# Kernel optimization log

Hardware: AMD Instinct MI355X
Metric: run time of the kernel (lower is better)

Reference implementation:

```python
import jax, jax.numpy as jnp
import numpy as np

B = 8192
T = 100       # repeat_vector
I = 30        # input_size
H = 100       # hidden_size


def setup_inputs() -> dict:
    key = jax.random.key(0)
    ks = jax.random.split(key, 7)
    k = 1.0 / np.sqrt(H)  # torch LSTM/Linear init scale
    u = lambda kk, shape: jax.random.uniform(kk, shape, jnp.float32, -k, k)
    return {
        "x": jax.random.normal(ks[0], (B, I), jnp.float32),
        "W_ih": u(ks[1], (4 * H, I)),   # gate order: i, f, g, o
        "W_hh": u(ks[2], (4 * H, H)),
        "b_ih": u(ks[3], (4 * H,)),
        "b_hh": u(ks[4], (4 * H,)),
        "W_d": u(ks[5], (1, H)),
        "b_d": u(ks[6], (1,)),
    }


def _lstm_dense(x, W_ih, W_hh, b_ih, b_hh, W_d, b_d):
    # Input is the same vector at every timestep (repeat), so project once.
    xp = x @ W_ih.T + b_ih + b_hh  # [B, 4H]
    h0 = jnp.zeros((x.shape[0], H), x.dtype)
    c0 = jnp.zeros((x.shape[0], H), x.dtype)

    def step(carry, _):
        h, c = carry
        gates = xp + h @ W_hh.T                      # [B, 4H]
        i, f, g, o = jnp.split(gates, 4, axis=-1)
        i = jax.nn.sigmoid(i)
        f = jax.nn.sigmoid(f)
        g = jnp.tanh(g)
        o = jax.nn.sigmoid(o)
        c = f * c + i * g
        h = o * jnp.tanh(c)
        return (h, c), h

    _, hs = jax.lax.scan(step, (h0, c0), None, length=T)  # [T, B, H]
    hs = jnp.transpose(hs, (1, 0, 2))                     # [B, T, H]
    return hs @ W_d.T + b_d                               # [B, T, 1]


def reference(x, W_ih, W_hh, b_ih, b_hh, W_d, b_d):
    return _lstm_dense(x, W_ih, W_hh, b_ih, b_hh, W_d, b_d)
```

## Files before the change

kernel.cpp:

```cpp
#include <hip/hip_runtime.h>


#define LOG2E 1.44269504088896340736f

typedef _Float16 f16x8 __attribute__((ext_vector_type(8)));
typedef float    f32x4 __attribute__((ext_vector_type(4)));
typedef float    f32x2 __attribute__((ext_vector_type(2)));

__device__ __forceinline__ float rcp_(float x) { return __builtin_amdgcn_rcpf(x); }
__device__ __forceinline__ float exp2_(float x) { return __builtin_amdgcn_exp2f(x); }

#define KS2 168

__global__ __launch_bounds__(448, 4) void lstm_kernel(
    const float* __restrict__ x, const float* __restrict__ Wih,
    const float* __restrict__ Whh, const float* __restrict__ bih,
    const float* __restrict__ bhh, const float* __restrict__ Wd,
    const float* __restrict__ bd, float* __restrict__ out)
{
    __shared__ __align__(16) char smem[128 * KS2 * 2];
    __shared__ __align__(16) _Float16 hlds[2][16 * KS2];

    _Float16* Wstg = (_Float16*)smem;
    float*    outb = (float*)smem;

    const int tid = threadIdx.x;
    const int w   = tid >> 6;
    const int l   = tid & 63;
    const int g   = l >> 4;
    const int c   = l & 15;
    const int b0  = blockIdx.x * 16;
    const int u   = w * 16 + c;
    const bool wpo = (w == 6) && (c == 5);

    for (int i = tid; i < 128 * KS2 / 2; i += 448) ((unsigned*)Wstg)[i] = 0u;
    for (int i = tid; i < 2 * 16 * KS2 / 2; i += 448) ((unsigned*)&hlds[0][0])[i] = 0u;
    __syncthreads();

    for (int idx = tid; idx < 960; idx += 448) {
        int buf = idx / 480, rem = idx - buf * 480;
        int rr = rem / 30, kk = rem - rr * 30;
        hlds[buf][rr * KS2 + 112 + kk] = (_Float16)x[(b0 + rr) * 30 + kk];
    }
    if (tid < 32) hlds[tid >> 4][(tid & 15) * KS2 + 142] = (_Float16)1.0f;

    f16x8 wfrag[4][5];
    for (int s = 0; s < 4; ++s) {
        const float sc = (s == 2) ? (-2.0f * LOG2E) : (-LOG2E);
        for (int idx = tid; idx < 13100; idx += 448) {
            if (idx < 10000) {
                int uu = idx / 100, k = idx - uu * 100;
                Wstg[uu * KS2 + k] = (_Float16)(Whh[(s * 100 + uu) * 100 + k] * sc);
            } else if (idx < 13000) {
                int j = idx - 10000, uu = j / 30, k = j - uu * 30;
                Wstg[uu * KS2 + 112 + k] = (_Float16)(Wih[(s * 100 + uu) * 30 + k] * sc);
            } else {
                int uu = idx - 13000;
                Wstg[uu * KS2 + 142] =
                    (_Float16)((bih[s * 100 + uu] + bhh[s * 100 + uu]) * sc);
            }
        }
        if (s == 0) {
            for (int k = tid; k < 100; k += 448)
                Wstg[101 * KS2 + k] = (_Float16)Wd[k];
            if (tid == 0) Wstg[101 * KS2 + 142] = (_Float16)bd[0];
        }
        __syncthreads();
        #pragma unroll
        for (int ks = 0; ks < 5; ++ks)
            wfrag[s][ks] = *(const f16x8*)&Wstg[u * KS2 + ks * 32 + g * 8];
        __syncthreads();
    }

    f32x2 creg2[2] = {{0.f, 0.f}, {0.f, 0.f}};
    __syncthreads();

    const int afb = c * KS2 + g * 8;

#define STEP(P, TCUR)                                                         \
    {                                                                         \
        const _Float16* hr = &hlds[(P)][0];                                   \
        _Float16*       hw = &hlds[(P) ^ 1][0];                               \
        f32x4 acc[4];                                                         \
        _Pragma("unroll")                                                     \
        for (int s = 0; s < 4; ++s) acc[s] = (f32x4){0.f, 0.f, 0.f, 0.f};     \
        _Pragma("unroll")                                                     \
        for (int ks = 0; ks < 5; ++ks) {                                      \
            f16x8 a = *(const f16x8*)&hr[afb + ks * 32];                      \
            _Pragma("unroll")                                                 \
            for (int s = 0; s < 4; ++s)                                       \
                acc[s] = __builtin_amdgcn_mfma_f32_16x16x32_f16(              \
                        a, wfrag[s][ks], acc[s], 0, 0, 0);                    \
        }                                                                     \
              \
        if ((TCUR) > 0 && wpo) {                                              \
            _Pragma("unroll")                                                 \
            for (int r = 0; r < 4; ++r)                                       \
                outb[(4 * g + r) * 100 + (TCUR) - 1] = acc[0][r];             \
        }                                                                     \
                                   \
        _Pragma("unroll")                                                     \
        for (int q = 0; q < 2; ++q) {                                         \
            f32x2 A2 = {exp2_(acc[0][2 * q]), exp2_(acc[0][2 * q + 1])};      \
            f32x2 F2 = {exp2_(acc[1][2 * q]), exp2_(acc[1][2 * q + 1])};      \
            f32x2 G2 = {exp2_(acc[2][2 * q]), exp2_(acc[2][2 * q + 1])};      \
            f32x2 O2 = {exp2_(acc[3][2 * q]), exp2_(acc[3][2 * q + 1])};      \
            f32x2 a1 = A2 + 1.0f;                                             \
            f32x2 f1 = F2 + 1.0f;                                             \
            f32x2 g1 = G2 + 1.0f;                                             \
            f32x2 gm = 1.0f - G2;                                             \
            f32x2 ag = a1 * g1;                                               \
            f32x2 num = creg2[q] * ag + gm * f1;                              \
            f32x2 den = ag * f1;                                              \
            f32x2 rd = {rcp_(den[0]), rcp_(den[1])};                          \
            f32x2 cg = num * rd;                                              \
            creg2[q] = cg;                                                    \
            f32x2 cgk = cg * (-2.0f * LOG2E);                                 \
            f32x2 C2 = {exp2_(cgk[0]), exp2_(cgk[1])};                        \
            f32x2 c2m = 1.0f - C2;                                            \
            f32x2 od = (O2 + 1.0f) * (C2 + 1.0f);                             \
            f32x2 ro = {rcp_(od[0]), rcp_(od[1])};                            \
            f32x2 hv = c2m * ro;                                              \
            hw[(4 * g + 2 * q) * KS2 + u]     = (_Float16)hv[0];              \
            hw[(4 * g + 2 * q + 1) * KS2 + u] = (_Float16)hv[1];              \
        }                                                                     \
        __syncthreads();                                                      \
    }

    for (int t2 = 0; t2 < 50; ++t2) {
        STEP(0, 2 * t2);
        STEP(1, 2 * t2 + 1);
    }
#undef STEP

    {
        f32x4 a99 = {0.f, 0.f, 0.f, 0.f};
        #pragma unroll
        for (int ks = 0; ks < 5; ++ks) {
            f16x8 a = *(const f16x8*)&hlds[0][afb + ks * 32];
            a99 = __builtin_amdgcn_mfma_f32_16x16x32_f16(a, wfrag[0][ks], a99, 0, 0, 0);
        }
        if (wpo) {
            #pragma unroll
            for (int r = 0; r < 4; ++r)
                outb[(4 * g + r) * 100 + 99] = a99[r];
        }
    }
    __syncthreads();

    {
        f32x4*       o4 = (f32x4*)(out + b0 * 100);
        const f32x4* s4 = (const f32x4*)outb;
        for (int i = tid; i < 400; i += 448) o4[i] = s4[i];
    }
}

extern "C" void kernel_launch(void* const* d_in, const int* in_sizes, int n_in,
                              void* d_out, int out_size, void* d_ws, size_t ws_size,
                              hipStream_t stream) {
    (void)in_sizes; (void)n_in; (void)out_size; (void)d_ws; (void)ws_size;
    const float* x   = (const float*)d_in[0];
    const float* Wih = (const float*)d_in[1];
    const float* Whh = (const float*)d_in[2];
    const float* bih = (const float*)d_in[3];
    const float* bhh = (const float*)d_in[4];
    const float* Wd  = (const float*)d_in[5];
    const float* bd  = (const float*)d_in[6];
    lstm_kernel<<<dim3(512), dim3(448), 0, stream>>>(
        x, Wih, Whh, bih, bhh, Wd, bd, (float*)d_out);
}
```

Before: 154.3 us.

## Precompute input projection once in fp32 and seed MFMA accumulators from LDS

The fp16 input columns (x, bias, constant one) no longer ride inside every recurrent MFMA. The time-invariant input projection x·W_ih + bias is now computed once per unit in fp32, stored in LDS, and reloaded each step as the initial accumulator. This cuts the K dimension from 5 to 4 MFMA slices per gate per step and shrinks the LDS row stride. The cost is an extra LDS read of 16 floats per thread per step and a scalar setup loop over 30 inputs. The dense bias is now added in fp32 instead of through the MFMA.

```diff
diff --git a/kernel.cpp b/kernel.cpp
--- a/kernel.cpp
+++ b/kernel.cpp
@@ -10,7 +10,8 @@
 __device__ __forceinline__ float rcp_(float x) { return __builtin_amdgcn_rcpf(x); }
 __device__ __forceinline__ float exp2_(float x) { return __builtin_amdgcn_exp2f(x); }
 
-#define KS2 168
+#define KS 136
+#define XQR 288
 
 __global__ __launch_bounds__(448, 4) void lstm_kernel(
     const float* __restrict__ x, const float* __restrict__ Wih,
@@ -18,8 +19,9 @@
     const float* __restrict__ bhh, const float* __restrict__ Wd,
     const float* __restrict__ bd, float* __restrict__ out)
 {
-    __shared__ __align__(16) char smem[128 * KS2 * 2];
-    __shared__ __align__(16) _Float16 hlds[2][16 * KS2];
+    __shared__ __align__(16) char smem[128 * KS * 2];
+    __shared__ __align__(16) _Float16 hlds[2][16 * KS];
+    __shared__ __align__(16) float xq_lds[7 * 4 * XQR];
 
     _Float16* Wstg = (_Float16*)smem;
     float*    outb = (float*)smem;
@@ -31,72 +33,94 @@
     const int c   = l & 15;
     const int b0  = blockIdx.x * 16;
     const int u   = w * 16 + c;
-    const bool wpo = (w == 6) && (c == 5);
+    const bool wpo = (u == 101);
 
-    for (int i = tid; i < 128 * KS2 / 2; i += 448) ((unsigned*)Wstg)[i] = 0u;
-    for (int i = tid; i < 2 * 16 * KS2 / 2; i += 448) ((unsigned*)&hlds[0][0])[i] = 0u;
+    for (int i = tid; i < 128 * KS / 2; i += 448) ((unsigned*)Wstg)[i] = 0u;
+    for (int i = tid; i < 2 * 16 * KS / 2; i += 448) ((unsigned*)&hlds[0][0])[i] = 0u;
     __syncthreads();
 
-    for (int idx = tid; idx < 960; idx += 448) {
-        int buf = idx / 480, rem = idx - buf * 480;
-        int rr = rem / 30, kk = rem - rr * 30;
-        hlds[buf][rr * KS2 + 112 + kk] = (_Float16)x[(b0 + rr) * 30 + kk];
-    }
-    if (tid < 32) hlds[tid >> 4][(tid & 15) * KS2 + 142] = (_Float16)1.0f;
-
-    f16x8 wfrag[4][5];
+    f16x8 wfrag[4][4];
     for (int s = 0; s < 4; ++s) {
         const float sc = (s == 2) ? (-2.0f * LOG2E) : (-LOG2E);
-        for (int idx = tid; idx < 13100; idx += 448) {
-            if (idx < 10000) {
-                int uu = idx / 100, k = idx - uu * 100;
-                Wstg[uu * KS2 + k] = (_Float16)(Whh[(s * 100 + uu) * 100 + k] * sc);
-            } else if (idx < 13000) {
-                int j = idx - 10000, uu = j / 30, k = j - uu * 30;
-                Wstg[uu * KS2 + 112 + k] = (_Float16)(Wih[(s * 100 + uu) * 30 + k] * sc);
-            } else {
-                int uu = idx - 13000;
-                Wstg[uu * KS2 + 142] =
-                    (_Float16)((bih[s * 100 + uu] + bhh[s * 100 + uu]) * sc);
-            }
+        for (int idx = tid; idx < 10000; idx += 448) {
+            int uu = idx / 100, k = idx - uu * 100;
+            Wstg[uu * KS + k] = (_Float16)(Whh[(s * 100 + uu) * 100 + k] * sc);
         }
-        if (s == 0) {
+        if (s == 0)
             for (int k = tid; k < 100; k += 448)
-                Wstg[101 * KS2 + k] = (_Float16)Wd[k];
-            if (tid == 0) Wstg[101 * KS2 + 142] = (_Float16)bd[0];
-        }
+                Wstg[101 * KS + k] = (_Float16)Wd[k];
         __syncthreads();
         #pragma unroll
-        for (int ks = 0; ks < 5; ++ks)
-            wfrag[s][ks] = *(const f16x8*)&Wstg[u * KS2 + ks * 32 + g * 8];
+        for (int ks = 0; ks < 4; ++ks)
+            wfrag[s][ks] = *(const f16x8*)&Wstg[u * KS + ks * 32 + g * 8];
         __syncthreads();
     }
 
+    const int xqsw = l * 4 + ((l >> 3) << 2);
+    {
+        float xq[4][4];
+        #pragma unroll
+        for (int s = 0; s < 4; ++s)
+            #pragma unroll
+            for (int r = 0; r < 4; ++r) xq[s][r] = 0.0f;
+        if (u < 100) {
+            for (int k = 0; k < 30; ++k) {
+                float xv[4];
+                #pragma unroll
+                for (int r = 0; r < 4; ++r) xv[r] = x[(b0 + 4 * g + r) * 30 + k];
+                #pragma unroll
+                for (int s = 0; s < 4; ++s) {
+                    float wv = Wih[(s * 100 + u) * 30 + k];
+                    #pragma unroll
+                    for (int r = 0; r < 4; ++r) xq[s][r] += xv[r] * wv;
+                }
+            }
+            #pragma unroll
+            for (int s = 0; s < 4; ++s) {
+                float sc = (s == 2) ? (-2.0f * LOG2E) : (-LOG2E);
+                float b  = bih[s * 100 + u] + bhh[s * 100 + u];
+                #pragma unroll
+                for (int r = 0; r < 4; ++r) xq[s][r] = (xq[s][r] + b) * sc;
+            }
+        }
+        #pragma unroll
+        for (int s = 0; s < 4; ++s) {
+            f32x4 v = {xq[s][0], xq[s][1], xq[s][2], xq[s][3]};
+            *(f32x4*)&xq_lds[(w * 4 + s) * XQR + xqsw] = v;
+        }
+    }
+    const float bdv = bd[0];
     f32x2 creg2[2] = {{0.f, 0.f}, {0.f, 0.f}};
     __syncthreads();
 
-    const int afb = c * KS2 + g * 8;
+    const int afb = c * KS + g * 8;
+    const int xqb = w * 4 * XQR + xqsw;
+
+    f32x4 acc[4];
+    #pragma unroll
+    for (int s = 0; s < 4; ++s)
+        acc[s] = *(const f32x4*)&xq_lds[xqb + s * XQR];
+    __syncthreads();
 
 #define STEP(P, TCUR)                                                         \
     {                                                                         \
         const _Float16* hr = &hlds[(P)][0];                                   \
         _Float16*       hw = &hlds[(P) ^ 1][0];                               \
-        f32x4 acc[4];                                                         \
+        f16x8 af[4];                                                          \
         _Pragma("unroll")                                                     \
-        for (int s = 0; s < 4; ++s) acc[s] = (f32x4){0.f, 0.f, 0.f, 0.f};     \
+        for (int ks = 0; ks < 4; ++ks)                                        \
+            af[ks] = *(const f16x8*)&hr[afb + ks * 32];                       \
         _Pragma("unroll")                                                     \
-        for (int ks = 0; ks < 5; ++ks) {                                      \
-            f16x8 a = *(const f16x8*)&hr[afb + ks * 32];                      \
+        for (int ks = 0; ks < 4; ++ks)                                        \
             _Pragma("unroll")                                                 \
             for (int s = 0; s < 4; ++s)                                       \
                 acc[s] = __builtin_amdgcn_mfma_f32_16x16x32_f16(              \
-                        a, wfrag[s][ks], acc[s], 0, 0, 0);                    \
-        }                                                                     \
-              \
+                        af[ks], wfrag[s][ks], acc[s], 0, 0, 0);               \
+                  \
         if ((TCUR) > 0 && wpo) {                                              \
             _Pragma("unroll")                                                 \
             for (int r = 0; r < 4; ++r)                                       \
-                outb[(4 * g + r) * 100 + (TCUR) - 1] = acc[0][r];             \
+                outb[(4 * g + r) * 100 + (TCUR) - 1] = acc[0][r] + bdv;       \
         }                                                                     \
                                    \
         _Pragma("unroll")                                                     \
@@ -121,9 +145,13 @@
             f32x2 od = (O2 + 1.0f) * (C2 + 1.0f);                             \
             f32x2 ro = {rcp_(od[0]), rcp_(od[1])};                            \
             f32x2 hv = c2m * ro;                                              \
-            hw[(4 * g + 2 * q) * KS2 + u]     = (_Float16)hv[0];              \
-            hw[(4 * g + 2 * q + 1) * KS2 + u] = (_Float16)hv[1];              \
+            hw[(4 * g + 2 * q) * KS + u]     = (_Float16)hv[0];               \
+            hw[(4 * g + 2 * q + 1) * KS + u] = (_Float16)hv[1];               \
         }                                                                     \
+                  \
+        _Pragma("unroll")                                                     \
+        for (int s = 0; s < 4; ++s)                                           \
+            acc[s] = *(const f32x4*)&xq_lds[xqb + s * XQR];                   \
         __syncthreads();                                                      \
     }
 
@@ -136,14 +164,14 @@
     {
         f32x4 a99 = {0.f, 0.f, 0.f, 0.f};
         #pragma unroll
-        for (int ks = 0; ks < 5; ++ks) {
+        for (int ks = 0; ks < 4; ++ks) {
             f16x8 a = *(const f16x8*)&hlds[0][afb + ks * 32];
             a99 = __builtin_amdgcn_mfma_f32_16x16x32_f16(a, wfrag[0][ks], a99, 0, 0, 0);
         }
         if (wpo) {
             #pragma unroll
             for (int r = 0; r < 4; ++r)
-                outb[(4 * g + r) * 100 + 99] = a99[r];
+                outb[(4 * g + r) * 100 + 99] = a99[r] + bdv;
         }
     }
     __syncthreads();
```

Result: faster. 138.7 us (median of 2 runs) (-10.1%).
